# Kernel tuning notes

Measured on AMD Instinct MI355X. Metric: run time of the kernel, lower is better.

The kernel has to match this reference:

```python
import jax, jax.numpy as jnp
import numpy as np

V, H, B, T_ENC, S, T_DEC, G = 18000, 400, 16, 256, 30, 8, 3


def setup_inputs() -> dict:
    key = jax.random.key(0)
    ks = jax.random.split(key, 16)
    def n(k, shape, s=0.1):
        return jax.random.normal(k, shape, jnp.float32) * s
    return {
        'story': jax.random.randint(ks[0], (B, T_ENC), 0, V, dtype=jnp.int32),
        'target_batches': jax.random.randint(ks[1], (B, S, T_DEC), 0, V, dtype=jnp.int32),
        'emb': n(ks[2], (V, H)),
        'enc_Wih_f': n(ks[3], (3 * H, H)), 'enc_Whh_f': n(ks[4], (3 * H, H)),
        'enc_bih_f': jnp.zeros((3 * H,), jnp.float32), 'enc_bhh_f': jnp.zeros((3 * H,), jnp.float32),
        'enc_Wih_b': n(ks[5], (3 * H, H)), 'enc_Whh_b': n(ks[6], (3 * H, H)),
        'enc_bih_b': jnp.zeros((3 * H,), jnp.float32), 'enc_bhh_b': jnp.zeros((3 * H,), jnp.float32),
        'dec_Wih': n(ks[7], (3 * H, H)), 'dec_Whh': n(ks[8], (3 * H, H)),
        'dec_bih': jnp.zeros((3 * H,), jnp.float32), 'dec_bhh': jnp.zeros((3 * H,), jnp.float32),
        'W_ratio': n(ks[9], (1, 3 * H)), 'b_ratio': jnp.zeros((1,), jnp.float32),
        'W_gate': n(ks[10], (G, H)), 'b_gate': jnp.zeros((G,), jnp.float32),
        'slot_emb': n(ks[11], (S, H)),
    }


def _gru_step(h, x, Wih, Whh, bih, bhh):
    # PyTorch GRU gate order: r, z, n
    gi = x @ Wih.T + bih
    gh = h @ Whh.T + bhh
    ir, iz, ig = jnp.split(gi, 3, axis=-1)
    hr, hz, hg = jnp.split(gh, 3, axis=-1)
    r = jax.nn.sigmoid(ir + hr)
    z = jax.nn.sigmoid(iz + hz)
    g = jnp.tanh(ig + r * hg)
    return (1.0 - z) * g + z * h


def _run_gru(xs, h0, Wih, Whh, bih, bhh):
    def step(h, x):
        h2 = _gru_step(h, x, Wih, Whh, bih, bhh)
        return h2, h2
    hT, out = jax.lax.scan(step, h0, xs)
    return out, hT


def reference(story, target_batches, emb,
              enc_Wih_f, enc_Whh_f, enc_bih_f, enc_bhh_f,
              enc_Wih_b, enc_Whh_b, enc_bih_b, enc_bhh_b,
              dec_Wih, dec_Whh, dec_bih, dec_bhh,
              W_ratio, b_ratio, W_gate, b_gate, slot_emb):
    # ---- EncoderRNN (bidirectional 1-layer GRU; dropout=0 / eval mode) ----
    x = emb[story.T]                       # (T_enc, B, H)
    h0 = jnp.zeros((B, H), x.dtype)
    out_f, h_f = _run_gru(x, h0, enc_Wih_f, enc_Whh_f, enc_bih_f, enc_bhh_f)
    out_b_rev, h_b = _run_gru(x[::-1], h0, enc_Wih_b, enc_Whh_b, enc_bih_b, enc_bhh_b)
    out_b = out_b_rev[::-1]
    enc_out = jnp.transpose(out_f + out_b, (1, 0, 2))   # (B, T_enc, H) = fwd+bwd halves summed
    enc_hidden = h_f + h_b                               # (B, H)     = hidden[0] + hidden[1]

    # ---- Generator decode loop ----
    SB = S * B
    dec_in0 = jnp.broadcast_to(slot_emb[:, None, :], (S, B, H)).reshape(SB, H)
    h = jnp.tile(enc_hidden, (S, 1))                     # (SB, H)
    enc_tiled = jnp.tile(enc_out, (S, 1, 1))             # (SB, T_enc, H)
    story_tiled = jnp.tile(story, (S, 1))                # (SB, T_enc)
    rows = jnp.arange(SB)[:, None]
    # teacher-forcing tokens per step, slot-major flatten to (T_dec, SB)
    tf_tokens = jnp.transpose(target_batches, (2, 1, 0)).reshape(T_DEC, SB)

    def step(carry, tok):
        h, dec_in = carry
        h2 = _gru_step(h, dec_in, dec_Wih, dec_Whh, dec_bih, dec_bhh)  # dec_state == new hidden
        scores = jnp.einsum('nd,ntd->nt', h2, enc_tiled)               # attend (all lens == T_enc)
        prob = jax.nn.softmax(scores, axis=1)
        context = jnp.einsum('nt,ntd->nd', prob, enc_tiled)
        gate = context @ W_gate.T + b_gate                              # (SB, G)
        p_vocab = jax.nn.softmax(h2 @ emb.T, axis=1)                    # (SB, V)
        p_gen = jnp.concatenate([h2, context, dec_in], axis=-1)         # (SB, 3H)
        sw = jax.nn.sigmoid(p_gen @ W_ratio.T + b_ratio)                # (SB, 1)
        ptr = jnp.zeros((SB, V), prob.dtype).at[rows, story_tiled].add(prob)  # scatter_add copy dist
        final = (1.0 - sw) * ptr + sw * p_vocab
        dec_in_next = emb[tok]                                          # teacher forcing
        return (h2, dec_in_next), (final, gate)

    _, (finals, gates) = jax.lax.scan(step, (h, dec_in0), tf_tokens)
    all_pointer_outputs = finals.reshape(T_DEC, S, B, V).transpose(1, 2, 0, 3)  # (S, B, T_dec, V)
    all_gate_outputs = gates[0].reshape(S, B, G)                                 # gate from step 0
    return all_pointer_outputs, all_gate_outputs
```

## Files before the change

kernel.cpp:

```cpp
#include <hip/hip_runtime.h>
#include <cstdint>
#include <cstddef>

#define VV 18000
#define HH 400
#define H3 1200
#define H3P 1280
#define KP 416
#define BB 16
#define TE 256
#define SS 30
#define TDN 8
#define GGN 3
#define SBN 480
#define NROW_ENC 4096
#define VP 18048
#define MP_DEC 512

#define EBLK 25

typedef __bf16 bf16;
typedef __attribute__((ext_vector_type(8))) __bf16 bf16x8;
typedef __attribute__((ext_vector_type(4))) float f32x4;
typedef __attribute__((ext_vector_type(4))) unsigned int u32x4;

static __device__ __forceinline__ float sigf(float x) {
    return 1.0f / (1.0f + __expf(-x));
}

__global__ __launch_bounds__(256) void gemm_bt(const bf16* __restrict__ A,
                                               const bf16* __restrict__ B,
                                               float* __restrict__ C,
                                               int M, int N, int K) {
    __shared__ __align__(16) bf16 sA[128 * 32];
    __shared__ __align__(16) bf16 sB[128 * 32];
    const int tid = threadIdx.x;
    const int lane = tid & 63;
    const int wave = tid >> 6;
    const int wm = wave >> 1, wn = wave & 1;
    const int m0 = blockIdx.x * 128, n0 = blockIdx.y * 128;
    f32x4 acc[4][4] = {};
    const int c0 = tid, c1 = tid + 256;
    const int r0 = c0 >> 2, q0 = (c0 & 3) * 8;
    const int r1 = c1 >> 2, q1 = (c1 & 3) * 8;
    const int ar = lane & 15, ak = (lane >> 4) * 8;
    const int nk = K >> 5;
    for (int kt = 0; kt < nk; ++kt) {
        const int kb = kt * 32;
        uint4 a0 = *(const uint4*)(A + (size_t)(m0 + r0) * K + kb + q0);
        uint4 a1 = *(const uint4*)(A + (size_t)(m0 + r1) * K + kb + q1);
        uint4 b0 = *(const uint4*)(B + (size_t)(n0 + r0) * K + kb + q0);
        uint4 b1 = *(const uint4*)(B + (size_t)(n0 + r1) * K + kb + q1);
        __syncthreads();
        *(uint4*)(sA + r0 * 32 + q0) = a0;
        *(uint4*)(sA + r1 * 32 + q1) = a1;
        *(uint4*)(sB + r0 * 32 + q0) = b0;
        *(uint4*)(sB + r1 * 32 + q1) = b1;
        __syncthreads();
        bf16x8 af[4], bg[4];
#pragma unroll
        for (int i = 0; i < 4; ++i)
            af[i] = *(const bf16x8*)(sA + (wm * 64 + i * 16 + ar) * 32 + ak);
#pragma unroll
        for (int j = 0; j < 4; ++j)
            bg[j] = *(const bf16x8*)(sB + (wn * 64 + j * 16 + ar) * 32 + ak);
#pragma unroll
        for (int i = 0; i < 4; ++i)
#pragma unroll
            for (int j = 0; j < 4; ++j)
                acc[i][j] = __builtin_amdgcn_mfma_f32_16x16x32_bf16(af[i], bg[j], acc[i][j], 0, 0, 0);
    }
    const int cr = (lane >> 4) * 4, cc = lane & 15;
#pragma unroll
    for (int i = 0; i < 4; ++i)
#pragma unroll
        for (int j = 0; j < 4; ++j)
#pragma unroll
            for (int q = 0; q < 4; ++q) {
                int row = m0 + wm * 64 + i * 16 + cr + q;
                int col = n0 + wn * 64 + j * 16 + cc;
                C[(size_t)row * N + col] = acc[i][j][q];
            }
}

__global__ void prep_pad_bf16(const float* __restrict__ src, bf16* __restrict__ dst,
                              int rows_real, int cols_real, int rows_pad, int cols_pad) {
    int idx = blockIdx.x * blockDim.x + threadIdx.x;
    int total = rows_pad * cols_pad;
    if (idx >= total) return;
    int r = idx / cols_pad, c = idx % cols_pad;
    float v = (r < rows_real && c < cols_real) ? src[(size_t)r * cols_real + c] : 0.f;
    dst[idx] = (bf16)v;
}

__global__ void prep_aenc(const int* __restrict__ story, const float* __restrict__ emb,
                          bf16* __restrict__ dst) {
    int idx = blockIdx.x * blockDim.x + threadIdx.x;
    if (idx >= NROW_ENC * KP) return;
    int m = idx / KP, k = idx % KP;
    int t = m >> 4, b = m & 15;
    float v = 0.f;
    if (k < HH) {
        int tok = story[b * TE + t];
        v = emb[(size_t)tok * HH + k];
    }
    dst[idx] = (bf16)v;
}

__global__ void prep_decx(const int* __restrict__ target, const float* __restrict__ emb,
                          const float* __restrict__ slot, float* __restrict__ xf,
                          bf16* __restrict__ xb) {
    int idx = blockIdx.x * blockDim.x + threadIdx.x;
    if (idx >= TDN * SBN * KP) return;
    int k = idx % KP;
    int nn = idx / KP;
    int n = nn % SBN;
    int td = nn / SBN;
    int s = n >> 4, b = n & 15;
    float v = 0.f;
    if (k < HH) {
        if (td == 0) v = slot[s * HH + k];
        else {
            int tok = target[(b * SS + s) * TDN + (td - 1)];
            v = emb[(size_t)tok * HH + k];
        }
        xf[((size_t)td * SBN + n) * HH + k] = v;
    }
    xb[idx] = (bf16)v;
}

__global__ void zero_bf16k(bf16* dst, size_t total) {
    size_t idx = (size_t)blockIdx.x * blockDim.x + threadIdx.x;
    if (idx < total) dst[idx] = (bf16)0.f;
}

__global__ __launch_bounds__(256) void enc_rnn10(
    const float* __restrict__ gi_f, const float* __restrict__ gi_b,
    const float* __restrict__ whh_f, const float* __restrict__ whh_b,
    const float* __restrict__ bih_f, const float* __restrict__ bhh_f,
    const float* __restrict__ bih_b, const float* __restrict__ bhh_b,
    float* __restrict__ hist_f, float* __restrict__ hist_b,
    unsigned int* __restrict__ hbuf_f, unsigned int* __restrict__ hbuf_b,
    unsigned int* __restrict__ flags) {
    const int dir = blockIdx.x & 1;
    const int blk = blockIdx.x >> 1;
    const int j0 = blk * 16;
    const float* gi  = dir ? gi_b : gi_f;
    const float* whh = dir ? whh_b : whh_f;
    const float* bih = dir ? bih_b : bih_f;
    const float* bhh = dir ? bhh_b : bhh_f;
    float* hist = dir ? hist_b : hist_f;
    unsigned int* hbuf = dir ? hbuf_b : hbuf_f;

    __shared__ float GHL[3 * 256];

    const int tid = threadIdx.x;
    const int wv = tid >> 6, lane = tid & 63;

    const int ub = tid >> 4, ucol = tid & 15;
    const int uj = j0 + ucol;
    const float bihr = bih[uj], bihz = bih[HH + uj], bihg = bih[2 * HH + uj];
    const float bhhr = bhh[uj], bhhz = bhh[HH + uj], bhhg = bhh[2 * HH + uj];

    const int kk0 = (lane >> 4) * 8;
    bf16x8 Bf[13];
    if (wv < 3) {
        const int brow = wv * HH + j0 + (lane & 15);
#pragma unroll
        for (int ks = 0; ks < 13; ++ks) {
            bf16x8 v;
#pragma unroll
            for (int e = 0; e < 8; ++e) {
                int k = kk0 + ks * 32 + e;
                v[e] = (k < HH) ? (bf16)whh[(size_t)brow * HH + k] : (bf16)0.f;
            }
            Bf[ks] = v;
        }
    }

    union UV { unsigned int d[4]; bf16x8 v; };

    float hp = 0.f;

    for (int s = 0; s < TE; ++s) {
        const int tt = dir ? (TE - 1 - s) : s;
        const float* gir = gi + ((size_t)tt * BB + ub) * H3P;
        float gi0 = gir[uj];
        float gi1 = gir[HH + uj];
        float gi2 = gir[2 * HH + uj];

        f32x4 acc0 = {}, acc1 = {};
        if (s > 0) {
            if (wv == 0) {
                const unsigned int* fl = flags + ((size_t)dir * TE + (s - 1)) * 32;
                while (true) {
                    unsigned f = 1u;
                    if (lane < EBLK)
                        asm volatile("global_load_dword %0, %1, off sc0 sc1"
                                     : "=v"(f) : "v"(fl + lane));
                    asm volatile("s_waitcnt vmcnt(0)" ::: "memory");
                    if (__all((int)(f != 0u))) break;
                }
            }
            __syncthreads();
            if (wv < 3) {
                const int ttp = dir ? (tt + 1) : (tt - 1);
                const unsigned int* hrow =
                    hbuf + ((size_t)ttp * BB + (lane & 15)) * KP + kk0;
                u32x4 ua[13], ubv[13];
#pragma unroll
                for (int ks = 0; ks < 13; ++ks) {
                    asm volatile("global_load_dwordx4 %0, %1, off offset:%c2 sc0 sc1"
                                 : "=v"(ua[ks]) : "v"(hrow), "n"(ks * 128));
                    asm volatile("global_load_dwordx4 %0, %1, off offset:%c2 sc0 sc1"
                                 : "=v"(ubv[ks]) : "v"(hrow), "n"(ks * 128 + 16));
                }
                asm volatile("s_waitcnt vmcnt(0)" ::: "memory");
                __builtin_amdgcn_sched_barrier(0);
#pragma unroll
                for (int ks = 0; ks < 13; ++ks) {
                    u32x4 a = ua[ks], b = ubv[ks];
                    UV ah, al;
                    ah.d[0] = (a.x & 0xffffu) | (a.y << 16);
                    ah.d[1] = (a.z & 0xffffu) | (a.w << 16);
                    ah.d[2] = (b.x & 0xffffu) | (b.y << 16);
                    ah.d[3] = (b.z & 0xffffu) | (b.w << 16);
                    al.d[0] = (a.x >> 16) | (a.y & 0xffff0000u);
                    al.d[1] = (a.z >> 16) | (a.w & 0xffff0000u);
                    al.d[2] = (b.x >> 16) | (b.y & 0xffff0000u);
                    al.d[3] = (b.z >> 16) | (b.w & 0xffff0000u);
                    acc0 = __builtin_amdgcn_mfma_f32_16x16x32_bf16(ah.v, Bf[ks], acc0, 0, 0, 0);
                    acc1 = __builtin_amdgcn_mfma_f32_16x16x32_bf16(al.v, Bf[ks], acc1, 0, 0, 0);
                }
            }
        }
        if (wv < 3) {
            f32x4 at = acc0 + acc1;
            const int cb0 = wv * 256 + ((lane >> 4) * 4) * 16 + (lane & 15);
            GHL[cb0]      = at[0];
            GHL[cb0 + 16] = at[1];
            GHL[cb0 + 32] = at[2];
            GHL[cb0 + 48] = at[3];
        }
        __syncthreads();

        float ghr = GHL[tid];
        float ghz = GHL[256 + tid];
        float ghg = GHL[512 + tid];
        float r = sigf(gi0 + bihr + ghr + bhhr);
        float z = sigf(gi1 + bihz + ghz + bhhz);
        float g = tanhf(gi2 + bihg + r * (ghg + bhhg));
        float hn = (1.f - z) * g + z * hp;
        hp = hn;
        hist[((size_t)tt * BB + ub) * HH + uj] = hn;
        bf16 hi = (bf16)hn;
        bf16 lo = (bf16)(hn - (float)hi);
        unsigned int pk = (unsigned int)__builtin_bit_cast(unsigned short, hi)
                        | ((unsigned int)__builtin_bit_cast(unsigned short, lo) << 16);
        unsigned int* hw = hbuf + ((size_t)tt * BB + ub) * KP + uj;
        asm volatile("global_store_dword %0, %1, off sc0 sc1" :: "v"(hw), "v"(pk) : "memory");

        asm volatile("s_waitcnt vmcnt(0)" ::: "memory");
        __syncthreads();
        if (tid == 0) {
            unsigned int one = 1u;
            unsigned int* fw = flags + ((size_t)dir * TE + s) * 32 + blk;
            asm volatile("global_store_dword %0, %1, off sc0 sc1" :: "v"(fw), "v"(one) : "memory");
        }
    }
}

__global__ void combine_enc(const float* __restrict__ hf, const float* __restrict__ hb,
                            float* __restrict__ enc_out) {
    int idx = blockIdx.x * blockDim.x + threadIdx.x;
    if (idx >= BB * TE * HH) return;
    int hcol = idx % HH;
    int t = (idx / HH) % TE;
    int b = idx / (HH * TE);
    size_t src = ((size_t)t * BB + b) * HH + hcol;
    enc_out[idx] = hf[src] + hb[src];
}

__global__ void init_hdec2(const float* __restrict__ hf, const float* __restrict__ hb,
                           float* __restrict__ hdec, bf16* __restrict__ h2b) {
    int idx = blockIdx.x * blockDim.x + threadIdx.x;
    if (idx >= SBN * HH) return;
    int hcol = idx % HH;
    int n = idx / HH;
    int b = n & 15;
    float v = hf[((size_t)(TE - 1) * BB + b) * HH + hcol] + hb[((size_t)b) * HH + hcol];
    hdec[idx] = v;
    h2b[(size_t)n * KP + hcol] = (bf16)v;
}

__global__ void gru_dec2(const float* __restrict__ gi, const float* __restrict__ gh,
                         const float* __restrict__ bih, const float* __restrict__ bhh,
                         const float* __restrict__ hprev, float* __restrict__ hnew,
                         bf16* __restrict__ h2b) {
    int idx = blockIdx.x * blockDim.x + threadIdx.x;
    if (idx >= SBN * HH) return;
    int n = idx / HH, j = idx % HH;
    const float* gir = gi + (size_t)n * H3P;
    const float* ghr = gh + (size_t)n * H3P;
    float r = sigf(gir[j] + bih[j] + ghr[j] + bhh[j]);
    float z = sigf(gir[HH + j] + bih[HH + j] + ghr[HH + j] + bhh[HH + j]);
    float g = tanhf(gir[2 * HH + j] + bih[2 * HH + j] + r * (ghr[2 * HH + j] + bhh[2 * HH + j]));
    float hn = (1.f - z) * g + z * hprev[idx];
    hnew[idx] = hn;
    h2b[(size_t)n * KP + j] = (bf16)hn;
}

__global__ __launch_bounds__(256) void attn3(
    const float* __restrict__ hfall,
    const float* __restrict__ enc,
    const float* __restrict__ decxf,
    const float* __restrict__ Wr, const float* __restrict__ br,
    const float* __restrict__ Wg, const float* __restrict__ bg,
    float* __restrict__ probw,
    float* __restrict__ sww,
    float* __restrict__ outg) {
    const int b = blockIdx.x >> 1;
    const int half = blockIdx.x & 1;
    const int td = blockIdx.y;
    const int s0 = half * 15;
    const int tid = threadIdx.x;
    const int lane = tid & 63, wv = tid >> 6;

    __shared__ __align__(16) float h2L[15][HH];
    __shared__ __align__(16) float scL[15][TE];
    __shared__ __align__(16) float cxL[15][HH];

    const float* h2base = hfall + (size_t)(td + 1) * SBN * HH;
    for (int i = tid; i < 15 * HH; i += 256) {
        int j = i / HH, k = i % HH;
        int n = (s0 + j) * BB + b;
        h2L[j][k] = h2base[(size_t)n * HH + k];
    }
    __syncthreads();

    {
        float acc[15];
#pragma unroll
        for (int j = 0; j < 15; ++j) acc[j] = 0.f;
        const float4* er = (const float4*)(enc + ((size_t)b * TE + tid) * HH);
        for (int k4 = 0; k4 < HH / 4; ++k4) {
            float4 e = er[k4];
#pragma unroll
            for (int j = 0; j < 15; ++j) {
                float4 hv = *(const float4*)(&h2L[j][k4 * 4]);
                acc[j] += e.x * hv.x + e.y * hv.y + e.z * hv.z + e.w * hv.w;
            }
        }
#pragma unroll
        for (int j = 0; j < 15; ++j) scL[j][tid] = acc[j];
    }
    __syncthreads();

    for (int j = wv; j < 15; j += 4) {
        float v0 = scL[j][lane], v1 = scL[j][lane + 64];
        float v2 = scL[j][lane + 128], v3 = scL[j][lane + 192];
        float m = fmaxf(fmaxf(v0, v1), fmaxf(v2, v3));
        for (int d = 32; d; d >>= 1) m = fmaxf(m, __shfl_xor(m, d));
        v0 = __expf(v0 - m); v1 = __expf(v1 - m);
        v2 = __expf(v2 - m); v3 = __expf(v3 - m);
        float s = v0 + v1 + v2 + v3;
        for (int d = 32; d; d >>= 1) s += __shfl_xor(s, d);
        float inv = 1.f / s;
        scL[j][lane]       = v0 * inv;
        scL[j][lane + 64]  = v1 * inv;
        scL[j][lane + 128] = v2 * inv;
        scL[j][lane + 192] = v3 * inv;
    }
    __syncthreads();

    for (int i = tid; i < 15 * TE; i += 256) {
        int j = i / TE, t = i % TE;
        int n = (s0 + j) * BB + b;
        probw[((size_t)td * SBN + n) * TE + t] = scL[j][t];
    }

    {
        float cx0[15], cx1[15];
#pragma unroll
        for (int j = 0; j < 15; ++j) { cx0[j] = 0.f; cx1[j] = 0.f; }
        const int c0 = tid, c1 = tid + 256;
        const bool has2 = (c1 < HH);
        for (int t = 0; t < TE; t += 2) {
            const float* e0r = enc + ((size_t)b * TE + t) * HH;
            const float* e1r = e0r + HH;
            float e00 = e0r[c0], e01 = e1r[c0];
            float e10 = 0.f, e11 = 0.f;
            if (has2) { e10 = e0r[c1]; e11 = e1r[c1]; }
#pragma unroll
            for (int j = 0; j < 15; ++j) {
                float2 p = *(const float2*)(&scL[j][t]);
                cx0[j] += p.x * e00 + p.y * e01;
                cx1[j] += p.x * e10 + p.y * e11;
            }
        }
#pragma unroll
        for (int j = 0; j < 15; ++j) {
            cxL[j][c0] = cx0[j];
            if (has2) cxL[j][c1] = cx1[j];
        }
    }
    __syncthreads();

    for (int j = wv; j < 15; j += 4) {
        int n = (s0 + j) * BB + b;
        const float* dx = decxf + ((size_t)td * SBN + n) * HH;
        float a = 0.f;
        for (int k = lane; k < H3; k += 64) {
            float v = (k < HH) ? h2L[j][k]
                    : (k < 2 * HH) ? cxL[j][k - HH]
                    : dx[k - 2 * HH];
            a += v * Wr[k];
        }
        for (int d = 32; d; d >>= 1) a += __shfl_xor(a, d);
        if (lane == 0) sww[(size_t)td * SBN + n] = sigf(a + br[0]);
    }

    if (td == 0) {
        for (int j = wv; j < 15; j += 4) {
            int n = (s0 + j) * BB + b;
#pragma unroll
            for (int g = 0; g < GGN; ++g) {
                float a = 0.f;
                for (int k = lane; k < HH; k += 64) a += cxL[j][k] * Wg[g * HH + k];
                for (int d = 32; d; d >>= 1) a += __shfl_xor(a, d);
                if (lane == 0) outg[n * GGN + g] = a + bg[g];
            }
        }
    }
}

__global__ __launch_bounds__(1024) void smax_scatter2(
    const float* __restrict__ logits, const float* __restrict__ sw,
    const int* __restrict__ story, const float* __restrict__ probw,
    float* __restrict__ out, int td0) {
    int n = blockIdx.x, tid = threadIdx.x;
    int td = td0 + blockIdx.y;
    const float* lrow = logits + ((size_t)blockIdx.y * MP_DEC + n) * VP;
    const float* prow = probw + ((size_t)td * SBN + n) * TE;
    float swv = sw[(size_t)td * SBN + n];
    __shared__ float red[16];
    __shared__ float bc[2];
    float v[18];
    float mx = -1e30f;
#pragma unroll
    for (int i = 0; i < 18; ++i) {
        int c = tid + (i << 10);
        v[i] = (c < VV) ? lrow[c] : -1e30f;
        mx = fmaxf(mx, v[i]);
    }
    for (int d = 32; d; d >>= 1) mx = fmaxf(mx, __shfl_xor(mx, d));
    if ((tid & 63) == 0) red[tid >> 6] = mx;
    __syncthreads();
    if (tid == 0) {
        float m2 = red[0];
        for (int w = 1; w < 16; ++w) m2 = fmaxf(m2, red[w]);
        bc[0] = m2;
    }
    __syncthreads();
    mx = bc[0];
    float s = 0.f;
#pragma unroll
    for (int i = 0; i < 18; ++i) {
        int c = tid + (i << 10);
        if (c < VV) { v[i] = __expf(v[i] - mx); s += v[i]; }
    }
    for (int d = 32; d; d >>= 1) s += __shfl_xor(s, d);
    if ((tid & 63) == 0) red[tid >> 6] = s;
    __syncthreads();
    if (tid == 0) {
        float s2 = 0.f;
        for (int w = 0; w < 16; ++w) s2 += red[w];
        bc[1] = s2;
    }
    __syncthreads();
    float scale = swv / bc[1];
    float* orow = out + ((size_t)n * TDN + td) * VV;
#pragma unroll
    for (int i = 0; i < 18; ++i) {
        int c = tid + (i << 10);
        if (c < VV) orow[c] = v[i] * scale;
    }
    __syncthreads();
    if (tid < TE) {
        int b = n & 15;
        int tok = story[b * TE + tid];
        float val = (1.f - swv) * prow[tid];
        atomicAdd(orow + tok, val);
    }
}

static inline int cdiv(long long a, long long b) { return (int)((a + b - 1) / b); }

extern "C" void kernel_launch(void* const* d_in, const int* in_sizes, int n_in,
                              void* d_out, int out_size, void* d_ws, size_t ws_size,
                              hipStream_t stream) {
    const int*   story  = (const int*)d_in[0];
    const int*   target = (const int*)d_in[1];
    const float* emb    = (const float*)d_in[2];
    const float* wih_f  = (const float*)d_in[3];
    const float* whh_f  = (const float*)d_in[4];
    const float* bih_f  = (const float*)d_in[5];
    const float* bhh_f  = (const float*)d_in[6];
    const float* wih_b  = (const float*)d_in[7];
    const float* whh_b  = (const float*)d_in[8];
    const float* bih_b  = (const float*)d_in[9];
    const float* bhh_b  = (const float*)d_in[10];
    const float* dwih   = (const float*)d_in[11];
    const float* dwhh   = (const float*)d_in[12];
    const float* dbih   = (const float*)d_in[13];
    const float* dbhh   = (const float*)d_in[14];
    const float* wr     = (const float*)d_in[15];
    const float* brr    = (const float*)d_in[16];
    const float* wgg    = (const float*)d_in[17];
    const float* bgg    = (const float*)d_in[18];
    const float* slot   = (const float*)d_in[19];
    float* out = (float*)d_out;

    char* wsb = (char*)d_ws;
    size_t off = 0;
    auto alloc = [&](size_t bytes) -> char* {
        char* p = wsb + off;
        off = (off + bytes + 255) & ~(size_t)255;
        return p;
    };
    bf16*  embb  = (bf16*)alloc((size_t)VP * KP * 2);
    bf16*  aenc  = (bf16*)alloc((size_t)NROW_ENC * KP * 2);
    bf16*  wfb   = (bf16*)alloc((size_t)H3P * KP * 2);
    bf16*  wbb   = (bf16*)alloc((size_t)H3P * KP * 2);
    bf16*  dwihb = (bf16*)alloc((size_t)H3P * KP * 2);
    bf16*  dwhhb = (bf16*)alloc((size_t)H3P * KP * 2);
    bf16*  decxb = (bf16*)alloc((size_t)TDN * SBN * KP * 2);
    bf16*  h2ball= (bf16*)alloc((size_t)9 * MP_DEC * KP * 2);
    unsigned int* hbuff = (unsigned int*)alloc((size_t)TE * BB * KP * 4);
    unsigned int* hbufb = (unsigned int*)alloc((size_t)TE * BB * KP * 4);
    unsigned int* flags = (unsigned int*)alloc((size_t)2 * TE * 32 * 4);
    float* gif   = (float*)alloc((size_t)NROW_ENC * H3P * 4);
    float* gib   = (float*)alloc((size_t)NROW_ENC * H3P * 4);
    float* gidec = (float*)alloc((size_t)TDN * SBN * H3P * 4);
    float* ghdec = (float*)alloc((size_t)MP_DEC * H3P * 4);
    float* histf = (float*)alloc((size_t)TE * BB * HH * 4);
    float* histb = (float*)alloc((size_t)TE * BB * HH * 4);
    float* encout= (float*)alloc((size_t)BB * TE * HH * 4);
    float* decxf = (float*)alloc((size_t)TDN * SBN * HH * 4);
    float* hfall = (float*)alloc((size_t)9 * SBN * HH * 4);
    float* probw = (float*)alloc((size_t)TDN * SBN * TE * 4);
    float* sww   = (float*)alloc((size_t)TDN * SBN * 4);
    float* logits= (float*)alloc((size_t)MP_DEC * VP * 4);
    const size_t bigBytes = (size_t)TDN * MP_DEC * VP * 4;
    float* logitsAll = nullptr;
    if (off + bigBytes + 256 <= ws_size) logitsAll = (float*)alloc(bigBytes);
    (void)in_sizes; (void)n_in; (void)out_size;

    (void)hipMemsetAsync(flags, 0, (size_t)2 * TE * 32 * 4, stream);

    const int thr = 256;
    prep_pad_bf16<<<cdiv((long long)VP * KP, thr), thr, 0, stream>>>(emb, embb, VV, HH, VP, KP);
    prep_aenc<<<cdiv((long long)NROW_ENC * KP, thr), thr, 0, stream>>>(story, emb, aenc);
    prep_pad_bf16<<<cdiv((long long)H3P * KP, thr), thr, 0, stream>>>(wih_f, wfb, H3, HH, H3P, KP);
    prep_pad_bf16<<<cdiv((long long)H3P * KP, thr), thr, 0, stream>>>(wih_b, wbb, H3, HH, H3P, KP);
    prep_pad_bf16<<<cdiv((long long)H3P * KP, thr), thr, 0, stream>>>(dwih, dwihb, H3, HH, H3P, KP);
    prep_pad_bf16<<<cdiv((long long)H3P * KP, thr), thr, 0, stream>>>(dwhh, dwhhb, H3, HH, H3P, KP);
    prep_decx<<<cdiv((long long)TDN * SBN * KP, thr), thr, 0, stream>>>(target, emb, slot, decxf, decxb);
    zero_bf16k<<<cdiv((long long)9 * MP_DEC * KP, thr), thr, 0, stream>>>(h2ball, (size_t)9 * MP_DEC * KP);

    {
        dim3 g(NROW_ENC / 128, H3P / 128);
        gemm_bt<<<g, 256, 0, stream>>>(aenc, wfb, gif, NROW_ENC, H3P, KP);
        gemm_bt<<<g, 256, 0, stream>>>(aenc, wbb, gib, NROW_ENC, H3P, KP);
    }
    {
        dim3 g((TDN * SBN) / 128, H3P / 128);
        gemm_bt<<<g, 256, 0, stream>>>(decxb, dwihb, gidec, TDN * SBN, H3P, KP);
    }

    enc_rnn10<<<2 * EBLK, 256, 0, stream>>>(gif, gib, whh_f, whh_b,
                                            bih_f, bhh_f, bih_b, bhh_b,
                                            histf, histb, hbuff, hbufb, flags);

    combine_enc<<<cdiv((long long)BB * TE * HH, thr), thr, 0, stream>>>(histf, histb, encout);
    init_hdec2<<<cdiv((long long)SBN * HH, thr), thr, 0, stream>>>(histf, histb, hfall, h2ball);

    for (int td = 0; td < TDN; ++td) {
        dim3 g(MP_DEC / 128, H3P / 128);
        gemm_bt<<<g, 256, 0, stream>>>(h2ball + (size_t)td * MP_DEC * KP, dwhhb, ghdec,
                                       MP_DEC, H3P, KP);
        gru_dec2<<<cdiv((long long)SBN * HH, thr), thr, 0, stream>>>(
            gidec + (size_t)td * SBN * H3P, ghdec, dbih, dbhh,
            hfall + (size_t)td * SBN * HH,
            hfall + (size_t)(td + 1) * SBN * HH,
            h2ball + (size_t)(td + 1) * MP_DEC * KP);
    }

    {
        dim3 g(32, TDN);
        attn3<<<g, 256, 0, stream>>>(hfall, encout, decxf, wr, brr, wgg, bgg,
                                     probw, sww, out + (size_t)SBN * TDN * VV);
    }

    if (logitsAll) {
        dim3 g((TDN * MP_DEC) / 128, VP / 128);
        gemm_bt<<<g, 256, 0, stream>>>(h2ball + (size_t)MP_DEC * KP, embb, logitsAll,
                                       TDN * MP_DEC, VP, KP);
        dim3 gs(SBN, TDN);
        smax_scatter2<<<gs, 1024, 0, stream>>>(logitsAll, sww, story, probw, out, 0);
    } else {
        for (int td = 0; td < TDN; ++td) {
            dim3 g(MP_DEC / 128, VP / 128);
            gemm_bt<<<g, 256, 0, stream>>>(h2ball + (size_t)(td + 1) * MP_DEC * KP, embb, logits,
                                           MP_DEC, VP, KP);
            dim3 gs(SBN, 1);
            smax_scatter2<<<gs, 1024, 0, stream>>>(logits, sww, story, probw, out, td);
        }
    }
}
```

Measured before the change: 1.774 ms.

## Overlap decoder input GEMM and embedding cast with encoder recurrence; store logits in bf16

The decoder input-projection GEMM and the embedding fp32-to-bf16 conversion now run as extra blocks inside the encoder recurrence kernel. The recurrence occupies only 50 blocks, so the idle CUs can do this independent work while it runs. The vocabulary logits GEMM also writes bf16 instead of fp32, which halves the traffic of the large logits buffer read by the softmax/scatter kernel. The costs are reduced logit precision before the softmax, and the risk that the extra blocks delay scheduling of the spin-synchronised recurrence blocks.

```diff
diff --git a/kernel.cpp b/kernel.cpp
--- a/kernel.cpp
+++ b/kernel.cpp
@@ -18,6 +18,8 @@
 #define MP_DEC 512
 
 #define EBLK 25
+#define GIDEC_TILES 300
+#define EMBB_BLKS 256
 
 typedef __bf16 bf16;
 typedef __attribute__((ext_vector_type(8))) __bf16 bf16x8;
@@ -28,17 +30,15 @@
     return 1.0f / (1.0f + __expf(-x));
 }
 
-__global__ __launch_bounds__(256) void gemm_bt(const bf16* __restrict__ A,
-                                               const bf16* __restrict__ B,
-                                               float* __restrict__ C,
-                                               int M, int N, int K) {
+static __device__ void gemm_dev(const bf16* __restrict__ A, const bf16* __restrict__ B,
+                                float* __restrict__ Cf, bf16* __restrict__ Ch,
+                                int M, int N, int K, int m0, int n0) {
     __shared__ __align__(16) bf16 sA[128 * 32];
     __shared__ __align__(16) bf16 sB[128 * 32];
     const int tid = threadIdx.x;
     const int lane = tid & 63;
     const int wave = tid >> 6;
     const int wm = wave >> 1, wn = wave & 1;
-    const int m0 = blockIdx.x * 128, n0 = blockIdx.y * 128;
     f32x4 acc[4][4] = {};
     const int c0 = tid, c1 = tid + 256;
     const int r0 = c0 >> 2, q0 = (c0 & 3) * 8;
@@ -71,16 +71,36 @@
                 acc[i][j] = __builtin_amdgcn_mfma_f32_16x16x32_bf16(af[i], bg[j], acc[i][j], 0, 0, 0);
     }
     const int cr = (lane >> 4) * 4, cc = lane & 15;
-#pragma unroll
-    for (int i = 0; i < 4; ++i)
-#pragma unroll
-        for (int j = 0; j < 4; ++j)
-#pragma unroll
-            for (int q = 0; q < 4; ++q) {
-                int row = m0 + wm * 64 + i * 16 + cr + q;
-                int col = n0 + wn * 64 + j * 16 + cc;
-                C[(size_t)row * N + col] = acc[i][j][q];
-            }
+    if (Ch) {
+#pragma unroll
+        for (int i = 0; i < 4; ++i)
+#pragma unroll
+            for (int j = 0; j < 4; ++j)
+#pragma unroll
+                for (int q = 0; q < 4; ++q) {
+                    int row = m0 + wm * 64 + i * 16 + cr + q;
+                    int col = n0 + wn * 64 + j * 16 + cc;
+                    Ch[(size_t)row * N + col] = (bf16)acc[i][j][q];
+                }
+    } else {
+#pragma unroll
+        for (int i = 0; i < 4; ++i)
+#pragma unroll
+            for (int j = 0; j < 4; ++j)
+#pragma unroll
+                for (int q = 0; q < 4; ++q) {
+                    int row = m0 + wm * 64 + i * 16 + cr + q;
+                    int col = n0 + wn * 64 + j * 16 + cc;
+                    Cf[(size_t)row * N + col] = acc[i][j][q];
+                }
+    }
+}
+
+__global__ __launch_bounds__(256) void gemm_bt(const bf16* __restrict__ A,
+                                               const bf16* __restrict__ B,
+                                               float* __restrict__ Cf, bf16* __restrict__ Ch,
+                                               int M, int N, int K) {
+    gemm_dev(A, B, Cf, Ch, M, N, K, blockIdx.x * 128, blockIdx.y * 128);
 }
 
 __global__ void prep_pad_bf16(const float* __restrict__ src, bf16* __restrict__ dst,
@@ -134,16 +154,40 @@
     if (idx < total) dst[idx] = (bf16)0.f;
 }
 
-__global__ __launch_bounds__(256) void enc_rnn10(
+__global__ __launch_bounds__(256) void enc_fat(
     const float* __restrict__ gi_f, const float* __restrict__ gi_b,
     const float* __restrict__ whh_f, const float* __restrict__ whh_b,
     const float* __restrict__ bih_f, const float* __restrict__ bhh_f,
     const float* __restrict__ bih_b, const float* __restrict__ bhh_b,
     float* __restrict__ hist_f, float* __restrict__ hist_b,
     unsigned int* __restrict__ hbuf_f, unsigned int* __restrict__ hbuf_b,
-    unsigned int* __restrict__ flags) {
-    const int dir = blockIdx.x & 1;
-    const int blk = blockIdx.x >> 1;
+    unsigned int* __restrict__ flags,
+    const bf16* __restrict__ decxb, const bf16* __restrict__ dwihb,
+    float* __restrict__ gidec,
+    const float* __restrict__ emb, bf16* __restrict__ embb) {
+    const int bid = blockIdx.x;
+    const int tid = threadIdx.x;
+
+    if (bid >= 2 * EBLK) {
+        if (bid < 2 * EBLK + GIDEC_TILES) {
+            int t = bid - 2 * EBLK;
+            gemm_dev(decxb, dwihb, gidec, nullptr, TDN * SBN, H3P, KP,
+                     (t % 30) * 128, (t / 30) * 128);
+        } else {
+            const size_t total = (size_t)VP * KP;
+            size_t idx = (size_t)(bid - 2 * EBLK - GIDEC_TILES) * 256 + tid;
+            const size_t stride = (size_t)EMBB_BLKS * 256;
+            for (; idx < total; idx += stride) {
+                int r = (int)(idx / KP), c = (int)(idx % KP);
+                float v = (r < VV && c < HH) ? emb[(size_t)r * HH + c] : 0.f;
+                embb[idx] = (bf16)v;
+            }
+        }
+        return;
+    }
+
+    const int dir = bid & 1;
+    const int blk = bid >> 1;
     const int j0 = blk * 16;
     const float* gi  = dir ? gi_b : gi_f;
     const float* whh = dir ? whh_b : whh_f;
@@ -154,9 +198,7 @@
 
     __shared__ float GHL[3 * 256];
 
-    const int tid = threadIdx.x;
     const int wv = tid >> 6, lane = tid & 63;
-
     const int ub = tid >> 4, ucol = tid & 15;
     const int uj = j0 + ucol;
     const float bihr = bih[uj], bihz = bih[HH + uj], bihg = bih[2 * HH + uj];
@@ -434,13 +476,13 @@
     }
 }
 
-__global__ __launch_bounds__(1024) void smax_scatter2(
-    const float* __restrict__ logits, const float* __restrict__ sw,
+__global__ __launch_bounds__(1024) void smax_scatter3(
+    const bf16* __restrict__ logitsH, const float* __restrict__ sw,
     const int* __restrict__ story, const float* __restrict__ probw,
     float* __restrict__ out, int td0) {
     int n = blockIdx.x, tid = threadIdx.x;
     int td = td0 + blockIdx.y;
-    const float* lrow = logits + ((size_t)blockIdx.y * MP_DEC + n) * VP;
+    const bf16* lrow = logitsH + ((size_t)blockIdx.y * MP_DEC + n) * VP;
     const float* prow = probw + ((size_t)td * SBN + n) * TE;
     float swv = sw[(size_t)td * SBN + n];
     __shared__ float red[16];
@@ -450,7 +492,7 @@
 #pragma unroll
     for (int i = 0; i < 18; ++i) {
         int c = tid + (i << 10);
-        v[i] = (c < VV) ? lrow[c] : -1e30f;
+        v[i] = (c < VV) ? (float)lrow[c] : -1e30f;
         mx = fmaxf(mx, v[i]);
     }
     for (int d = 32; d; d >>= 1) mx = fmaxf(mx, __shfl_xor(mx, d));
@@ -550,16 +592,15 @@
     float* hfall = (float*)alloc((size_t)9 * SBN * HH * 4);
     float* probw = (float*)alloc((size_t)TDN * SBN * TE * 4);
     float* sww   = (float*)alloc((size_t)TDN * SBN * 4);
-    float* logits= (float*)alloc((size_t)MP_DEC * VP * 4);
-    const size_t bigBytes = (size_t)TDN * MP_DEC * VP * 4;
-    float* logitsAll = nullptr;
-    if (off + bigBytes + 256 <= ws_size) logitsAll = (float*)alloc(bigBytes);
+    bf16*  logitsH = (bf16*)alloc((size_t)MP_DEC * VP * 2);
+    const size_t bigBytes = (size_t)TDN * MP_DEC * VP * 2;
+    bf16* logitsAllH = nullptr;
+    if (off + bigBytes + 256 <= ws_size) logitsAllH = (bf16*)alloc(bigBytes);
     (void)in_sizes; (void)n_in; (void)out_size;
 
     (void)hipMemsetAsync(flags, 0, (size_t)2 * TE * 32 * 4, stream);
 
     const int thr = 256;
-    prep_pad_bf16<<<cdiv((long long)VP * KP, thr), thr, 0, stream>>>(emb, embb, VV, HH, VP, KP);
     prep_aenc<<<cdiv((long long)NROW_ENC * KP, thr), thr, 0, stream>>>(story, emb, aenc);
     prep_pad_bf16<<<cdiv((long long)H3P * KP, thr), thr, 0, stream>>>(wih_f, wfb, H3, HH, H3P, KP);
     prep_pad_bf16<<<cdiv((long long)H3P * KP, thr), thr, 0, stream>>>(wih_b, wbb, H3, HH, H3P, KP);
@@ -570,24 +611,21 @@
 
     {
         dim3 g(NROW_ENC / 128, H3P / 128);
-        gemm_bt<<<g, 256, 0, stream>>>(aenc, wfb, gif, NROW_ENC, H3P, KP);
-        gemm_bt<<<g, 256, 0, stream>>>(aenc, wbb, gib, NROW_ENC, H3P, KP);
-    }
-    {
-        dim3 g((TDN * SBN) / 128, H3P / 128);
-        gemm_bt<<<g, 256, 0, stream>>>(decxb, dwihb, gidec, TDN * SBN, H3P, KP);
-    }
-
-    enc_rnn10<<<2 * EBLK, 256, 0, stream>>>(gif, gib, whh_f, whh_b,
-                                            bih_f, bhh_f, bih_b, bhh_b,
-                                            histf, histb, hbuff, hbufb, flags);
+        gemm_bt<<<g, 256, 0, stream>>>(aenc, wfb, gif, nullptr, NROW_ENC, H3P, KP);
+        gemm_bt<<<g, 256, 0, stream>>>(aenc, wbb, gib, nullptr, NROW_ENC, H3P, KP);
+    }
+
+    enc_fat<<<2 * EBLK + GIDEC_TILES + EMBB_BLKS, 256, 0, stream>>>(
+        gif, gib, whh_f, whh_b, bih_f, bhh_f, bih_b, bhh_b,
+        histf, histb, hbuff, hbufb, flags,
+        decxb, dwihb, gidec, emb, embb);
 
     combine_enc<<<cdiv((long long)BB * TE * HH, thr), thr, 0, stream>>>(histf, histb, encout);
     init_hdec2<<<cdiv((long long)SBN * HH, thr), thr, 0, stream>>>(histf, histb, hfall, h2ball);
 
     for (int td = 0; td < TDN; ++td) {
         dim3 g(MP_DEC / 128, H3P / 128);
-        gemm_bt<<<g, 256, 0, stream>>>(h2ball + (size_t)td * MP_DEC * KP, dwhhb, ghdec,
+        gemm_bt<<<g, 256, 0, stream>>>(h2ball + (size_t)td * MP_DEC * KP, dwhhb, ghdec, nullptr,
                                        MP_DEC, H3P, KP);
         gru_dec2<<<cdiv((long long)SBN * HH, thr), thr, 0, stream>>>(
             gidec + (size_t)td * SBN * H3P, ghdec, dbih, dbhh,
@@ -602,19 +640,19 @@
                                      probw, sww, out + (size_t)SBN * TDN * VV);
     }
 
-    if (logitsAll) {
+    if (logitsAllH) {
         dim3 g((TDN * MP_DEC) / 128, VP / 128);
-        gemm_bt<<<g, 256, 0, stream>>>(h2ball + (size_t)MP_DEC * KP, embb, logitsAll,
+        gemm_bt<<<g, 256, 0, stream>>>(h2ball + (size_t)MP_DEC * KP, embb, nullptr, logitsAllH,
                                        TDN * MP_DEC, VP, KP);
         dim3 gs(SBN, TDN);
-        smax_scatter2<<<gs, 1024, 0, stream>>>(logitsAll, sww, story, probw, out, 0);
+        smax_scatter3<<<gs, 1024, 0, stream>>>(logitsAllH, sww, story, probw, out, 0);
     } else {
         for (int td = 0; td < TDN; ++td) {
             dim3 g(MP_DEC / 128, VP / 128);
-            gemm_bt<<<g, 256, 0, stream>>>(h2ball + (size_t)(td + 1) * MP_DEC * KP, embb, logits,
-                                           MP_DEC, VP, KP);
+            gemm_bt<<<g, 256, 0, stream>>>(h2ball + (size_t)(td + 1) * MP_DEC * KP, embb,
+                                           nullptr, logitsH, MP_DEC, VP, KP);
             dim3 gs(SBN, 1);
-            smax_scatter2<<<gs, 1024, 0, stream>>>(logits, sww, story, probw, out, td);
-        }
-    }
-}
+            smax_scatter3<<<gs, 1024, 0, stream>>>(logitsH, sww, story, probw, out, td);
+        }
+    }
+}
```

After: 1.710 ms, median of 2. 3.6% less time.
